# Kernel tuning notes

Hardware: AMD Instinct MI355X
Metric: run time of the kernel (lower is better)

The kernel has to match this reference:

```python
import jax, jax.numpy as jnp
import numpy as np

N_NODES = 50000
N_EDGES = 600000
CHANNELS = 128
HEADS = 8


def setup_inputs() -> dict:
    key = jax.random.key(0)
    k1, k2, k3 = jax.random.split(key, 3)
    x = jax.random.normal(k1, (N_NODES, CHANNELS), dtype=jnp.float32)
    edge_index = jax.random.randint(k2, (2, N_EDGES), 0, N_NODES, dtype=jnp.int32)
    att = jax.random.normal(k3, (HEADS, 2 * (CHANNELS // HEADS)), dtype=jnp.float32)
    return {"x": x, "edge_index": edge_index, "att": att}


def reference(x, edge_index, att):
    # x: [N, C], edge_index: [2, E], att: [H, 2*D] with D = C // H
    src, dst = edge_index[0], edge_index[1]
    n = x.shape[0]
    h = att.shape[0]
    d = att.shape[1] // 2

    x_src = x[src].reshape(-1, h, d)   # [E, H, D]
    x_dst = x[dst].reshape(-1, h, d)   # [E, H, D]

    # (cat([x_src, x_dst]) * att).sum(-1) == x_src @ att[:, :D] + x_dst @ att[:, D:]
    a_src, a_dst = att[:, :d], att[:, d:]
    alpha = jnp.einsum('ehd,hd->eh', x_src, a_src) + jnp.einsum('ehd,hd->eh', x_dst, a_dst)
    alpha = jnp.where(alpha >= 0, alpha, 0.2 * alpha)  # LeakyReLU(0.2)

    # segment softmax over dst; torch scatter_reduce amax includes the zero init,
    # so the per-node max is max(segment_max, 0)
    seg_max = jax.ops.segment_max(alpha, dst, num_segments=n)  # [N, H]
    seg_max = jnp.maximum(seg_max, 0.0)
    alpha = jnp.exp(alpha - seg_max[dst])
    seg_sum = jax.ops.segment_sum(alpha, dst, num_segments=n)  # [N, H]
    alpha = alpha / jnp.maximum(seg_sum[dst], 1e-10)

    # weighted scatter-add of source features
    weighted = x_src * alpha[..., None]                        # [E, H, D]
    out = jax.ops.segment_sum(weighted, dst, num_segments=n)   # [N, H, D]
    return out.reshape(n, -1)
```

## Files before the change

### kernel.cpp

```cpp
#include <hip/hip_runtime.h>

#define N_NODES  50000
#define N_EDGES  600000
#define CHANNELS 128
#define HEADS    8
#define HEAD_DIM 16
#define CAP      64
#define CSTRIDE  4

#define PREP_BLOCK 256
#define SCAT_GRID  ((N_EDGES + PREP_BLOCK - 1) / PREP_BLOCK)
#define LOGIT_GRID ((N_NODES * CHANNELS) / PREP_BLOCK)
#define WPB        4

__global__ void prep_kernel(const float* __restrict__ x,
                            const float* __restrict__ att,
                            const int*   __restrict__ src,
                            const int*   __restrict__ dst,
                            int*            __restrict__ cursor,
                            unsigned short* __restrict__ bucket,
                            float*          __restrict__ ls8,
                            float*          __restrict__ ld8,
                            unsigned short* __restrict__ xb) {
    int b = blockIdx.x;
    if (b < SCAT_GRID) {
        int e = b * PREP_BLOCK + threadIdx.x;
        if (e < N_EDGES) {
            int d = dst[e];
            int pos = atomicAdd(&cursor[d * CSTRIDE], 1);
            if (pos < CAP) bucket[(size_t)d * CAP + pos] = (unsigned short)src[e];
        }
    } else {
        int gid = (b - SCAT_GRID) * PREP_BLOCK + threadIdx.x;
        int n = gid >> 7;
        int c = gid & 127;
        int h = c >> 4;
        int j = c & 15;
        float v = x[gid];

        unsigned int u = __float_as_uint(v);
        xb[gid] = (unsigned short)((u + 0x7FFFu + ((u >> 16) & 1u)) >> 16);

        float ts = v * att[h * (2 * HEAD_DIM) + j];
        float td = v * att[h * (2 * HEAD_DIM) + HEAD_DIM + j];
#pragma unroll
        for (int o = 8; o >= 1; o >>= 1) {
            ts += __shfl_xor(ts, o, 16);
            td += __shfl_xor(td, o, 16);
        }
        if (j == 0) {
            ls8[n * HEADS + h] = ts;
            ld8[n * HEADS + h] = td;
        }
    }
}

__global__ void fused_gat_kernel(const unsigned short* __restrict__ xb,
                                 const float* __restrict__ ls8,
                                 const float* __restrict__ ld8,
                                 const int*   __restrict__ cursor,
                                 const unsigned short* __restrict__ bucket,
                                 float*       __restrict__ out) {
    __shared__ float s_a[WPB * CAP * HEADS];

    int wave = threadIdx.x >> 6;
    int lane = threadIdx.x & 63;
    int n = blockIdx.x * WPB + wave;
    if (n >= N_NODES) return;
    int h = lane >> 3;
    int j = lane & 7;

    int   cnt_raw = cursor[n * CSTRIDE];
    int   myidx   = (int)bucket[(size_t)n * CAP + lane];
    float ldst    = ld8[n * HEADS + h];
    int cnt = (cnt_raw > CAP) ? CAP : cnt_raw;

    float* sa = s_a + wave * (CAP * HEADS);

    float mymax = -1e30f;
    for (int i = j; i < cnt; i += 8) {
        int   s  = __shfl(myidx, i);
        float lg = ls8[s * HEADS + h] + ldst;
        float a  = (lg >= 0.0f) ? lg : 0.2f * lg;
        sa[i * HEADS + h] = a;
        mymax = fmaxf(mymax, a);
    }
#pragma unroll
    for (int o = 4; o >= 1; o >>= 1) mymax = fmaxf(mymax, __shfl_xor(mymax, o, 8));
    float m = fmaxf(mymax, 0.0f);

    float l = 0.0f, accx = 0.0f, accy = 0.0f;
    unsigned int q0 = 0, q1 = 0, q2 = 0;
    if (cnt > 0) {
        int s0 = __shfl(myidx, 0);
        q0 = ((const unsigned int*)(xb + (size_t)s0 * CHANNELS))[lane];
    }
    if (cnt > 1) {
        int s1 = __shfl(myidx, 1);
        q1 = ((const unsigned int*)(xb + (size_t)s1 * CHANNELS))[lane];
    }
    if (cnt > 2) {
        int s2 = __shfl(myidx, 2);
        q2 = ((const unsigned int*)(xb + (size_t)s2 * CHANNELS))[lane];
    }
    for (int i = 0; i < cnt; ++i) {
        unsigned int qc = q0;
        q0 = q1; q1 = q2;
        if (i + 3 < cnt) {
            int s3 = __shfl(myidx, i + 3);
            q2 = ((const unsigned int*)(xb + (size_t)s3 * CHANNELS))[lane];
        }
        float p  = __expf(sa[i * HEADS + h] - m);
        float cx = __uint_as_float(qc << 16);
        float cy = __uint_as_float(qc & 0xFFFF0000u);
        l    += p;
        accx += p * cx;
        accy += p * cy;
    }

    float inv = 1.0f / fmaxf(l, 1e-10f);
    *(float2*)(out + (size_t)n * CHANNELS + 2 * lane) =
        make_float2(accx * inv, accy * inv);
}

extern "C" void kernel_launch(void* const* d_in, const int* in_sizes, int n_in,
                              void* d_out, int out_size, void* d_ws, size_t ws_size,
                              hipStream_t stream) {
    const float* x   = (const float*)d_in[0];
    const int*   ei  = (const int*)  d_in[1];
    const float* att = (const float*)d_in[2];
    const int* src = ei;
    const int* dst = ei + N_EDGES;
    float* out = (float*)d_out;

    int*            cursor = (int*)d_ws;
    unsigned short* bucket = (unsigned short*)(cursor + (size_t)N_NODES * CSTRIDE);
    float*          ls8    = (float*)(bucket + (size_t)N_NODES * CAP);
    float*          ld8    = ls8 + (size_t)N_NODES * HEADS;
    unsigned short* xb     = (unsigned short*)(ld8 + (size_t)N_NODES * HEADS);

    hipMemsetAsync(cursor, 0, sizeof(int) * (size_t)N_NODES * CSTRIDE, stream);

    prep_kernel<<<SCAT_GRID + LOGIT_GRID, PREP_BLOCK, 0, stream>>>(
        x, att, src, dst, cursor, bucket, ls8, ld8, xb);

    {
        int grid = (N_NODES + WPB - 1) / WPB;
        fused_gat_kernel<<<grid, 64 * WPB, 0, stream>>>(
            xb, ls8, ld8, cursor, bucket, out);
    }
}
```

Measured before the change: 161.9 us.

## Merge memset, prep and aggregation into one cooperative persistent kernel

Result: slower. 495.7 us (+206.1%).

```diff
diff --git a/kernel.cpp b/kernel.cpp
--- a/kernel.cpp
+++ b/kernel.cpp
@@ -1,4 +1,7 @@
 #include <hip/hip_runtime.h>
+#include <hip/hip_cooperative_groups.h>
+
+namespace cg = cooperative_groups;
 
 #define N_NODES  50000
 #define N_EDGES  600000
@@ -6,121 +9,138 @@
 #define HEADS    8
 #define HEAD_DIM 16
 #define CAP      64
-#define CSTRIDE  4
+#define CSTRIDE  16
 
-#define PREP_BLOCK 256
-#define SCAT_GRID  ((N_EDGES + PREP_BLOCK - 1) / PREP_BLOCK)
-#define LOGIT_GRID ((N_NODES * CHANNELS) / PREP_BLOCK)
-#define WPB        4
+#define GRID   1024
+#define BLOCK  256
+#define WPB    4
 
-__global__ void prep_kernel(const float* __restrict__ x,
-                            const float* __restrict__ att,
-                            const int*   __restrict__ src,
-                            const int*   __restrict__ dst,
-                            int*            __restrict__ cursor,
-                            unsigned short* __restrict__ bucket,
-                            float*          __restrict__ ls8,
-                            float*          __restrict__ ld8,
-                            unsigned short* __restrict__ xb) {
-    int b = blockIdx.x;
-    if (b < SCAT_GRID) {
-        int e = b * PREP_BLOCK + threadIdx.x;
-        if (e < N_EDGES) {
-            int d = dst[e];
-            int pos = atomicAdd(&cursor[d * CSTRIDE], 1);
-            if (pos < CAP) bucket[(size_t)d * CAP + pos] = (unsigned short)src[e];
-        }
-    } else {
-        int gid = (b - SCAT_GRID) * PREP_BLOCK + threadIdx.x;
-        int n = gid >> 7;
-        int c = gid & 127;
-        int h = c >> 4;
-        int j = c & 15;
-        float v = x[gid];
+#define SCAT_VB  ((N_EDGES + BLOCK - 1) / BLOCK)
+#define LOGIT_VB ((N_NODES * CHANNELS) / BLOCK)
+#define AGG_VB   ((N_NODES + WPB - 1) / WPB)
+#define CUR_TOT  (N_NODES * CSTRIDE)
 
-        unsigned int u = __float_as_uint(v);
-        xb[gid] = (unsigned short)((u + 0x7FFFu + ((u >> 16) & 1u)) >> 16);
+__global__ __launch_bounds__(BLOCK, 4)
+void gat_all_kernel(const float* __restrict__ x,
+                    const float* __restrict__ att,
+                    const int*   __restrict__ src,
+                    const int*   __restrict__ dst,
+                    int*            __restrict__ cursor,
+                    unsigned short* __restrict__ bucket,
+                    float*          __restrict__ ls8,
+                    float*          __restrict__ ld8,
+                    unsigned short* __restrict__ xb,
+                    float*          __restrict__ out) {
+    cg::grid_group grid = cg::this_grid();
+    __shared__ float s_a[WPB * CAP * HEADS];
+    int tid = threadIdx.x;
 
-        float ts = v * att[h * (2 * HEAD_DIM) + j];
-        float td = v * att[h * (2 * HEAD_DIM) + HEAD_DIM + j];
+    for (int i = blockIdx.x * BLOCK + tid; i < CUR_TOT; i += GRID * BLOCK)
+        cursor[i] = 0;
+
+    __threadfence();
+    grid.sync();
+
+    for (int vb = blockIdx.x; vb < SCAT_VB + LOGIT_VB; vb += GRID) {
+        if (vb < SCAT_VB) {
+            int e = vb * BLOCK + tid;
+            if (e < N_EDGES) {
+                int d = dst[e];
+                int pos = atomicAdd(&cursor[d * CSTRIDE], 1);
+                if (pos < CAP) bucket[(size_t)d * CAP + pos] = (unsigned short)src[e];
+            }
+        } else {
+            int gid = (vb - SCAT_VB) * BLOCK + tid;
+            int n = gid >> 7;
+            int c = gid & 127;
+            int h = c >> 4;
+            int j = c & 15;
+            float v = x[gid];
+
+            unsigned int u = __float_as_uint(v);
+            xb[gid] = (unsigned short)((u + 0x7FFFu + ((u >> 16) & 1u)) >> 16);
+
+            float ts = v * att[h * (2 * HEAD_DIM) + j];
+            float td = v * att[h * (2 * HEAD_DIM) + HEAD_DIM + j];
 #pragma unroll
-        for (int o = 8; o >= 1; o >>= 1) {
-            ts += __shfl_xor(ts, o, 16);
-            td += __shfl_xor(td, o, 16);
-        }
-        if (j == 0) {
-            ls8[n * HEADS + h] = ts;
-            ld8[n * HEADS + h] = td;
+            for (int o = 8; o >= 1; o >>= 1) {
+                ts += __shfl_xor(ts, o, 16);
+                td += __shfl_xor(td, o, 16);
+            }
+            if (j == 0) {
+                ls8[n * HEADS + h] = ts;
+                ld8[n * HEADS + h] = td;
+            }
         }
     }
-}
 
-__global__ void fused_gat_kernel(const unsigned short* __restrict__ xb,
-                                 const float* __restrict__ ls8,
-                                 const float* __restrict__ ld8,
-                                 const int*   __restrict__ cursor,
-                                 const unsigned short* __restrict__ bucket,
-                                 float*       __restrict__ out) {
-    __shared__ float s_a[WPB * CAP * HEADS];
+    __threadfence();
+    grid.sync();
 
-    int wave = threadIdx.x >> 6;
-    int lane = threadIdx.x & 63;
-    int n = blockIdx.x * WPB + wave;
-    if (n >= N_NODES) return;
+    int wave = tid >> 6;
+    int lane = tid & 63;
     int h = lane >> 3;
     int j = lane & 7;
-
-    int   cnt_raw = cursor[n * CSTRIDE];
-    int   myidx   = (int)bucket[(size_t)n * CAP + lane];
-    float ldst    = ld8[n * HEADS + h];
-    int cnt = (cnt_raw > CAP) ? CAP : cnt_raw;
-
     float* sa = s_a + wave * (CAP * HEADS);
 
-    float mymax = -1e30f;
-    for (int i = j; i < cnt; i += 8) {
-        int   s  = __shfl(myidx, i);
-        float lg = ls8[s * HEADS + h] + ldst;
-        float a  = (lg >= 0.0f) ? lg : 0.2f * lg;
-        sa[i * HEADS + h] = a;
-        mymax = fmaxf(mymax, a);
+    for (int vb = blockIdx.x; vb < AGG_VB; vb += GRID) {
+        int n = vb * WPB + wave;
+
+        int   cnt_raw = cursor[n * CSTRIDE];
+        int   myidx   = (int)bucket[(size_t)n * CAP + lane];
+        float ldst    = ld8[n * HEADS + h];
+        int cnt = (cnt_raw > CAP) ? CAP : cnt_raw;
+
+        float mymax = -1e30f;
+        for (int i = j; i < cnt; i += 8) {
+            int   s  = __shfl(myidx, i);
+            float lg = ls8[s * HEADS + h] + ldst;
+            float a  = (lg >= 0.0f) ? lg : 0.2f * lg;
+            sa[i * HEADS + h] = a;
+            mymax = fmaxf(mymax, a);
+        }
+#pragma unroll
+        for (int o = 4; o >= 1; o >>= 1) mymax = fmaxf(mymax, __shfl_xor(mymax, o, 8));
+        float m = fmaxf(mymax, 0.0f);
+
+#define LQ(k) (((k) < cnt) ? ((const unsigned int*)(xb + (size_t)__shfl(myidx,(k)) * CHANNELS))[lane] : 0u)
+        unsigned int q0 = LQ(0), q1 = LQ(1), q2 = LQ(2), q3 = LQ(3);
+        unsigned int q4 = LQ(4), q5 = LQ(5), q6 = LQ(6), q7 = LQ(7);
+
+        float l0 = 0.f, l1 = 0.f;
+        float ax0 = 0.f, ay0 = 0.f, ax1 = 0.f, ay1 = 0.f;
+        int i = 0;
+        for (; i + 4 <= cnt; i += 4) {
+            float p0 = __expf(sa[(i + 0) * HEADS + h] - m);
+            float p1 = __expf(sa[(i + 1) * HEADS + h] - m);
+            float p2 = __expf(sa[(i + 2) * HEADS + h] - m);
+            float p3 = __expf(sa[(i + 3) * HEADS + h] - m);
+            l0 += p0 + p2;
+            l1 += p1 + p3;
+            ax0 += p0 * __uint_as_float(q0 << 16);
+            ay0 += p0 * __uint_as_float(q0 & 0xFFFF0000u);
+            ax1 += p1 * __uint_as_float(q1 << 16);
+            ay1 += p1 * __uint_as_float(q1 & 0xFFFF0000u);
+            ax0 += p2 * __uint_as_float(q2 << 16);
+            ay0 += p2 * __uint_as_float(q2 & 0xFFFF0000u);
+            ax1 += p3 * __uint_as_float(q3 << 16);
+            ay1 += p3 * __uint_as_float(q3 & 0xFFFF0000u);
+            q0 = q4; q1 = q5; q2 = q6; q3 = q7;
+            q4 = LQ(i + 8); q5 = LQ(i + 9); q6 = LQ(i + 10); q7 = LQ(i + 11);
+        }
+        for (; i < cnt; ++i) {
+            float p = __expf(sa[i * HEADS + h] - m);
+            l0  += p;
+            ax0 += p * __uint_as_float(q0 << 16);
+            ay0 += p * __uint_as_float(q0 & 0xFFFF0000u);
+            q0 = q1; q1 = q2; q2 = q3;
+        }
+#undef LQ
+        float l   = l0 + l1;
+        float inv = 1.0f / fmaxf(l, 1e-10f);
+        *(float2*)(out + (size_t)n * CHANNELS + 2 * lane) =
+            make_float2((ax0 + ax1) * inv, (ay0 + ay1) * inv);
     }
-#pragma unroll
-    for (int o = 4; o >= 1; o >>= 1) mymax = fmaxf(mymax, __shfl_xor(mymax, o, 8));
-    float m = fmaxf(mymax, 0.0f);
-
-    float l = 0.0f, accx = 0.0f, accy = 0.0f;
-    unsigned int q0 = 0, q1 = 0, q2 = 0;
-    if (cnt > 0) {
-        int s0 = __shfl(myidx, 0);
-        q0 = ((const unsigned int*)(xb + (size_t)s0 * CHANNELS))[lane];
-    }
-    if (cnt > 1) {
-        int s1 = __shfl(myidx, 1);
-        q1 = ((const unsigned int*)(xb + (size_t)s1 * CHANNELS))[lane];
-    }
-    if (cnt > 2) {
-        int s2 = __shfl(myidx, 2);
-        q2 = ((const unsigned int*)(xb + (size_t)s2 * CHANNELS))[lane];
-    }
-    for (int i = 0; i < cnt; ++i) {
-        unsigned int qc = q0;
-        q0 = q1; q1 = q2;
-        if (i + 3 < cnt) {
-            int s3 = __shfl(myidx, i + 3);
-            q2 = ((const unsigned int*)(xb + (size_t)s3 * CHANNELS))[lane];
-        }
-        float p  = __expf(sa[i * HEADS + h] - m);
-        float cx = __uint_as_float(qc << 16);
-        float cy = __uint_as_float(qc & 0xFFFF0000u);
-        l    += p;
-        accx += p * cx;
-        accy += p * cy;
-    }
-
-    float inv = 1.0f / fmaxf(l, 1e-10f);
-    *(float2*)(out + (size_t)n * CHANNELS + 2 * lane) =
-        make_float2(accx * inv, accy * inv);
 }
 
 extern "C" void kernel_launch(void* const* d_in, const int* in_sizes, int n_in,
@@ -139,14 +159,9 @@
     float*          ld8    = ls8 + (size_t)N_NODES * HEADS;
     unsigned short* xb     = (unsigned short*)(ld8 + (size_t)N_NODES * HEADS);
 
-    hipMemsetAsync(cursor, 0, sizeof(int) * (size_t)N_NODES * CSTRIDE, stream);
-
-    prep_kernel<<<SCAT_GRID + LOGIT_GRID, PREP_BLOCK, 0, stream>>>(
-        x, att, src, dst, cursor, bucket, ls8, ld8, xb);
-
-    {
-        int grid = (N_NODES + WPB - 1) / WPB;
-        fused_gat_kernel<<<grid, 64 * WPB, 0, stream>>>(
-            xb, ls8, ld8, cursor, bucket, out);
-    }
+    void* args[] = { (void*)&x, (void*)&att, (void*)&src, (void*)&dst,
+                     (void*)&cursor, (void*)&bucket, (void*)&ls8, (void*)&ld8,
+                     (void*)&xb, (void*)&out };
+    hipLaunchCooperativeKernel((const void*)gat_all_kernel,
+                               dim3(GRID), dim3(BLOCK), args, 0, stream);
 }
```
